# Kernel optimization log

Measured on AMD Instinct MI355X. Metric: run time of the kernel, lower is better.

Reference implementation:

```python
import jax, jax.numpy as jnp
import numpy as np

B, H, W, C = 32, 56, 56, 256
NH, WS, SHIFT = 8, 7, 3
S = WS * WS            # tokens per window = 49
CH = C // NH           # channels per head = 32
EPS = 1e-5


def layer_norm(x, w, b):
    mu = jnp.mean(x, axis=-1, keepdims=True)
    var = jnp.var(x, axis=-1, keepdims=True)
    return (x - mu) * jax.lax.rsqrt(var + EPS) * w + b


def spatial_mlp(x, weight, bias):
    # x: (B, H*W, C); weight: (NH*S, S, 1) grouped-conv1d weight; bias: (NH*S,)
    xr = x.reshape(B, H, W, C)
    if SHIFT > 0:
        P_l, P_r, P_t, P_b = WS - SHIFT, SHIFT, WS - SHIFT, SHIFT
        xr = jnp.pad(xr, ((0, 0), (P_t, P_b), (P_l, P_r), (0, 0)))
    Hp, Wp = xr.shape[1], xr.shape[2]
    # window partition -> (nW, S, NH, CH)
    win = xr.reshape(B, Hp // WS, WS, Wp // WS, WS, C)
    win = win.transpose(0, 1, 3, 2, 4, 5).reshape(-1, S, NH, CH)
    # grouped 1x1 conv == per-head token-mixing matrix (S x S)
    wgt = weight.reshape(NH, S, S)             # wgt[h, i, j]
    out = jnp.einsum('hij,njhd->nihd', wgt, win)
    out = out + bias.reshape(NH, S).T[None, :, :, None]
    # window reverse -> (B, Hp, Wp, C)
    out = out.reshape(B, Hp // WS, Wp // WS, WS, WS, C)
    out = out.transpose(0, 1, 3, 2, 4, 5).reshape(B, Hp, Wp, C)
    if SHIFT > 0:
        out = out[:, P_t:Hp - P_b, P_l:Wp - P_r, :]
    return out.reshape(B, H * W, C)


def mlp(x, fc1_w, fc1_b, fc2_w, fc2_b):
    h = jax.nn.gelu(x @ fc1_w + fc1_b, approximate=False)
    return h @ fc2_w + fc2_b


def setup_inputs() -> dict:
    key = jax.random.key(0)
    ks = jax.random.split(key, 5)
    sc = 0.02
    return {
        'x': jax.random.normal(ks[0], (B, H * W, C), jnp.float32),
        'norm1_w': jnp.ones((C,), jnp.float32),
        'norm1_b': jnp.zeros((C,), jnp.float32),
        'spatial_w': jax.random.normal(ks[1], (NH * S, S, 1), jnp.float32) * sc,
        'spatial_b': jax.random.normal(ks[2], (NH * S,), jnp.float32) * sc,
        'norm2_w': jnp.ones((C,), jnp.float32),
        'norm2_b': jnp.zeros((C,), jnp.float32),
        'fc1_w': jax.random.normal(ks[3], (C, 4 * C), jnp.float32) * sc,
        'fc1_b': jnp.zeros((4 * C,), jnp.float32),
        'fc2_w': jax.random.normal(ks[4], (4 * C, C), jnp.float32) * sc,
        'fc2_b': jnp.zeros((C,), jnp.float32),
    }


def reference(x, norm1_w, norm1_b, spatial_w, spatial_b, norm2_w, norm2_b,
              fc1_w, fc1_b, fc2_w, fc2_b):
    shortcut = x
    h = layer_norm(x, norm1_w, norm1_b)
    h = spatial_mlp(h, spatial_w, spatial_b)
    x = shortcut + h                      # drop_path = 0 (eval)
    x = x + mlp(layer_norm(x, norm2_w, norm2_b), fc1_w, fc1_b, fc2_w, fc2_b)
    return x
```

## Files before the change

### kernel.cpp

```cpp
#include <hip/hip_runtime.h>
#include <hip/hip_bf16.h>

#define NHEAD 8
#define IMG   3136
#define MTOT  100352

typedef __attribute__((ext_vector_type(2))) _Float16 f16x2;
typedef __attribute__((ext_vector_type(8))) _Float16 f16x8;
typedef __attribute__((ext_vector_type(4))) float    f32x4;
typedef __attribute__((ext_vector_type(16))) float   f32x16;
typedef __attribute__((ext_vector_type(8))) short    bf16x8;
typedef __attribute__((ext_vector_type(4))) short    s16x4;
typedef __attribute__((ext_vector_type(4))) int      i32x4;

#define SWZA(byteoff, r) ((byteoff) ^ (((r)&7)<<4) ^ ((((r)>>3)&1)<<7))

__device__ __forceinline__ short f2bf(float f){
  union { float fv; unsigned u; } a; a.fv = f;
  unsigned u = a.u;
  unsigned r = (u + 0x7fffu + ((u >> 16) & 1u)) >> 16;
  return (short)r;
}

__device__ __forceinline__ float gelu_f(float v){
  float u = v*(0.7978845608028654f + 0.0356774081f*(v*v));
  float e = __expf(2.f*u);
  float th = 1.f - 2.f/(e + 1.f);
  return 0.5f*v*(1.f + th);
}

__global__ void prep_k(const float* __restrict__ fc1w, const float* __restrict__ fc2w,
                       const float* __restrict__ spw,
                       short* __restrict__ w1p, short* __restrict__ w2p,
                       short* __restrict__ wspA)
{
  int bid = blockIdx.x, t = threadIdx.x;
  if (bid < 128) {
    int id = bid*256 + t;
    int l = id & 63, fk = id >> 6;
    int kk = fk & 15, f = fk >> 4;
    int n = f*32 + (l & 31);
    int kbase = kk*16 + (l >> 5)*8;
    bf16x8 o;
    #pragma unroll
    for (int e = 0; e < 8; ++e) o[e] = f2bf(fc1w[(size_t)(kbase+e)*1024 + n]);
    *(bf16x8*)(w1p + (size_t)id*8) = o;
  } else if (bid < 256) {
    int id = (bid-128)*256 + t;
    int l = id & 63, fk = id >> 6;
    int kk = fk & 63, f = fk >> 6;
    int n = f*32 + (l & 31);
    int kbase = kk*16 + (l >> 5)*8;
    bf16x8 o;
    #pragma unroll
    for (int e = 0; e < 8; ++e) o[e] = f2bf(fc2w[(size_t)(kbase+e)*256 + n]);
    *(bf16x8*)(w2p + (size_t)id*8) = o;
  } else {
    #pragma unroll
    for (int k = 0; k < 16; ++k) {
      int idx = t + k*256;
      int lane = idx & 63;
      int kt = (idx >> 6) & 3;
      int mt = (idx >> 8) & 1;
      int h  = idx >> 9;
      int i  = mt*32 + (lane & 31);
      int jb = kt*16 + (lane >> 5)*8;
      bf16x8 o;
      #pragma unroll
      for (int e = 0; e < 8; ++e) {
        int j = jb + e;
        float v = (i < 49 && j < 49) ? spw[(size_t)(h*49 + i)*49 + j] : 0.f;
        o[e] = f2bf(v);
      }
      *(bf16x8*)(wspA + (size_t)idx*8) = o;
    }
  }
}

__global__ __launch_bounds__(512,4) void win_k(
    const float* __restrict__ x, const float* __restrict__ n1w, const float* __restrict__ n1b,
    const float* __restrict__ spb, const short* __restrict__ wspA,
    float* __restrict__ x1)
{
  extern __shared__ char wsm[];
  char*  lxT  = wsm;
  float* murs = (float*)(wsm + 65536);
  int t = threadIdx.x, lane = t & 63, wave = t >> 6;
  int bid = blockIdx.x;

  #pragma unroll
  for (int w = 0; w < 2; ++w) {
    int win = bid*2 + w;
    int b = win/81, rem = win - b*81, wi = rem/9, wj = rem - (rem/9)*9;
    for (int i = wave; i < 49; i += 8) {
      int iy = i/7, ix = i - iy*7;
      int hh = wi*7 + iy - 4, ww = wj*7 + ix - 4;
      if (hh < 0 || hh >= 56 || ww < 0 || ww >= 56) continue;
      const float* row = x + ((size_t)(b*IMG + hh*56 + ww))*256;
      f32x4 v = *(const f32x4*)(row + lane*4);
      float s  = v[0]+v[1]+v[2]+v[3];
      float s2 = v[0]*v[0]+v[1]*v[1]+v[2]*v[2]+v[3]*v[3];
      #pragma unroll
      for (int m = 1; m < 64; m <<= 1) { s += __shfl_xor(s, m); s2 += __shfl_xor(s2, m); }
      float mu = s * (1.f/256.f);
      float rs = rsqrtf(s2*(1.f/256.f) - mu*mu + 1e-5f);
      if (lane == 0) { murs[(w*56+i)*2] = mu; murs[(w*56+i)*2+1] = rs; }
    }
  }
  __syncthreads();

  {
    int w = t >> 8, c = t & 255;
    int win = bid*2 + w;
    int b = win/81, rem = win - b*81, wi = rem/9, wj = rem - (rem/9)*9;
    float nwc = n1w[c], nbc = n1b[c];
    char* rowb = lxT + c*256;
    #pragma unroll
    for (int cj = 0; cj < 7; ++cj) {
      bf16x8 pk;
      #pragma unroll
      for (int e = 0; e < 8; ++e) {
        int p = cj*8 + e;
        short val = 0;
        if (p < 49) {
          int iy = p/7, ix = p - iy*7;
          int hh = wi*7 + iy - 4, ww = wj*7 + ix - 4;
          if (hh >= 0 && hh < 56 && ww >= 0 && ww < 56) {
            float mu = murs[(w*56+p)*2], rs = murs[(w*56+p)*2+1];
            float xv = x[((size_t)(b*IMG + hh*56 + ww))*256 + c];
            val = f2bf((xv - mu)*rs*nwc + nbc);
          }
        }
        pk[e] = val;
      }
      *(bf16x8*)(rowb + SWZA(w*128 + cj*16, c)) = pk;
    }
    bf16x8 z = {0,0,0,0,0,0,0,0};
    *(bf16x8*)(rowb + SWZA(w*128 + 112, c)) = z;
  }
  __syncthreads();

  int h = wave, d = lane & 31, lk = lane >> 5;
  const short* wA = wspA + h*4096;
  int c = h*32 + d;
  f32x16 a00, a01, a10, a11;
  #pragma unroll
  for (int q = 0; q < 16; ++q) { a00[q]=0.f; a01[q]=0.f; a10[q]=0.f; a11[q]=0.f; }
  #pragma unroll
  for (int kt = 0; kt < 4; ++kt) {
    bf16x8 A0 = *(const bf16x8*)(wA + (kt*64 + lane)*8);
    bf16x8 A1 = *(const bf16x8*)(wA + ((4+kt)*64 + lane)*8);
    int bo = kt*32 + lk*16;
    bf16x8 B0 = *(const bf16x8*)(lxT + c*256 + SWZA(bo, c));
    bf16x8 B1 = *(const bf16x8*)(lxT + c*256 + SWZA(128 + bo, c));
    a00 = __builtin_amdgcn_mfma_f32_32x32x16_bf16(A0, B0, a00, 0,0,0);
    a10 = __builtin_amdgcn_mfma_f32_32x32x16_bf16(A1, B0, a10, 0,0,0);
    a01 = __builtin_amdgcn_mfma_f32_32x32x16_bf16(A0, B1, a01, 0,0,0);
    a11 = __builtin_amdgcn_mfma_f32_32x32x16_bf16(A1, B1, a11, 0,0,0);
  }

  #pragma unroll
  for (int w = 0; w < 2; ++w) {
    int win = bid*2 + w;
    int b = win/81, rem = win - b*81, wi = rem/9, wj = rem - (rem/9)*9;
    #pragma unroll
    for (int mt = 0; mt < 2; ++mt) {
      #pragma unroll
      for (int r = 0; r < 16; ++r) {
        int i = mt*32 + (r&3) + 8*(r>>2) + 4*lk;
        if (i < 49) {
          int iy = i/7, ix = i - iy*7;
          int hh = wi*7 + iy - 4, ww = wj*7 + ix - 4;
          if (hh >= 0 && hh < 56 && ww >= 0 && ww < 56) {
            size_t off = ((size_t)(b*IMG + hh*56 + ww))*256 + c;
            float av = mt==0 ? (w==0 ? a00[r] : a01[r]) : (w==0 ? a10[r] : a11[r]);
            x1[off] = x[off] + av + spb[h*49 + i];
          }
        }
      }
    }
  }
}

__global__ __launch_bounds__(512,4) void mlp_k(
    const float* __restrict__ x1, float* __restrict__ out,
    const short* __restrict__ w1p, const short* __restrict__ w2p,
    const float* __restrict__ n2w, const float* __restrict__ n2b,
    const float* __restrict__ b1, const float* __restrict__ b2)
{
  extern __shared__ char sm[];
  char* a2  = sm;
  char* hcb = sm + 32768;

  int t = threadIdx.x, lane = t & 63, wave = t >> 6;
  int m0 = blockIdx.x * 64;

  {
    f32x4 nw = *(const f32x4*)(n2w + lane*4);
    f32x4 nb = *(const f32x4*)(n2b + lane*4);
    #pragma unroll
    for (int rq = 0; rq < 8; ++rq) {
      int rr = wave*8 + rq;
      f32x4 v = *(const f32x4*)(x1 + (size_t)(m0+rr)*256 + lane*4);
      float s  = v[0]+v[1]+v[2]+v[3];
      float s2 = v[0]*v[0]+v[1]*v[1]+v[2]*v[2]+v[3]*v[3];
      #pragma unroll
      for (int m = 1; m < 64; m <<= 1){ s += __shfl_xor(s,m); s2 += __shfl_xor(s2,m); }
      float mu = s*(1.f/256.f);
      float rs = rsqrtf(s2*(1.f/256.f) - mu*mu + 1e-5f);
      s16x4 pk;
      #pragma unroll
      for (int q = 0; q < 4; ++q) pk[q] = f2bf((v[q]-mu)*rs*nw[q] + nb[q]);
      *(s16x4*)(a2 + SWZA(lane*8, rr) + rr*512) = pk;
    }
  }
  __syncthreads();

  int lr = lane & 31, lk = lane >> 5;
  int wn = wave;

  f32x16 accO[2];
  #pragma unroll
  for (int i=0;i<2;++i)
    #pragma unroll
    for (int q=0;q<16;++q) accO[i][q] = 0.f;

  for (int ch = 0; ch < 4; ++ch) {
    f32x16 accH[2];
    #pragma unroll
    for (int i=0;i<2;++i)
      #pragma unroll
      for (int q=0;q<16;++q) accH[i][q] = 0.f;

    const short* w1f = w1p + ((size_t)((ch*8 + wn)*16)*64 + lane)*8;
    bf16x8 bq[4];
    #pragma unroll
    for (int k = 0; k < 4; ++k) bq[k] = *(const bf16x8*)(w1f + (size_t)k*512);
    __builtin_amdgcn_s_setprio(1);
    #pragma unroll
    for (int kk = 0; kk < 16; ++kk) {
      bf16x8 b = bq[kk & 3];
      if (kk < 12) bq[kk & 3] = *(const bf16x8*)(w1f + (size_t)(kk+4)*512);
      int kb = kk*32 + lk*16;
      bf16x8 a0 = *(const bf16x8*)(a2 + SWZA(kb, lr) + lr*512);
      bf16x8 a1 = *(const bf16x8*)(a2 + SWZA(kb, 32+lr) + (32+lr)*512);
      accH[0] = __builtin_amdgcn_mfma_f32_32x32x16_bf16(a0, b, accH[0], 0,0,0);
      accH[1] = __builtin_amdgcn_mfma_f32_32x32x16_bf16(a1, b, accH[1], 0,0,0);
    }
    __builtin_amdgcn_s_setprio(0);

    {
      float b1v = b1[ch*256 + wn*32 + lr];
      int colb = (wn*32 + lr)*2;
      #pragma unroll
      for (int ms = 0; ms < 2; ++ms) {
        #pragma unroll
        for (int r = 0; r < 16; ++r) {
          int rowl = ms*32 + (r&3) + 8*(r>>2) + 4*lk;
          float g = gelu_f(accH[ms][r] + b1v);
          *(short*)(hcb + SWZA(colb, rowl) + rowl*512) = f2bf(g);
        }
      }
    }
    __syncthreads();

    const short* w2f = w2p + ((size_t)(wn*64 + ch*16)*64 + lane)*8;
    #pragma unroll
    for (int k = 0; k < 4; ++k) bq[k] = *(const bf16x8*)(w2f + (size_t)k*512);
    __builtin_amdgcn_s_setprio(1);
    #pragma unroll
    for (int kk = 0; kk < 16; ++kk) {
      bf16x8 b = bq[kk & 3];
      if (kk < 12) bq[kk & 3] = *(const bf16x8*)(w2f + (size_t)(kk+4)*512);
      int kb = kk*32 + lk*16;
      bf16x8 a0 = *(const bf16x8*)(hcb + SWZA(kb, lr) + lr*512);
      bf16x8 a1 = *(const bf16x8*)(hcb + SWZA(kb, 32+lr) + (32+lr)*512);
      accO[0] = __builtin_amdgcn_mfma_f32_32x32x16_bf16(a0, b, accO[0], 0,0,0);
      accO[1] = __builtin_amdgcn_mfma_f32_32x32x16_bf16(a1, b, accO[1], 0,0,0);
    }
    __builtin_amdgcn_s_setprio(0);
    __syncthreads();
  }

  {
    int col = wn*32 + lr;
    float b2v = b2[col];
    #pragma unroll
    for (int ms = 0; ms < 2; ++ms) {
      #pragma unroll
      for (int r = 0; r < 16; ++r) {
        int row = ms*32 + (r&3) + 8*(r>>2) + 4*lk;
        size_t off = (size_t)(m0 + row)*256 + col;
        out[off] = x1[off] + accO[ms][r] + b2v;
      }
    }
  }
}

extern "C" void kernel_launch(void* const* d_in, const int* in_sizes, int n_in,
                              void* d_out, int out_size, void* d_ws, size_t ws_size,
                              hipStream_t stream) {
  const float* x    = (const float*)d_in[0];
  const float* n1w  = (const float*)d_in[1];
  const float* n1b  = (const float*)d_in[2];
  const float* spw  = (const float*)d_in[3];
  const float* spb  = (const float*)d_in[4];
  const float* n2w  = (const float*)d_in[5];
  const float* n2b  = (const float*)d_in[6];
  const float* fc1w = (const float*)d_in[7];
  const float* fc1b = (const float*)d_in[8];
  const float* fc2w = (const float*)d_in[9];
  const float* fc2b = (const float*)d_in[10];
  float* outp = (float*)d_out;

  char* ws = (char*)d_ws;
  short* w1p  = (short*)ws;
  short* w2p  = (short*)(ws + 524288);
  short* wspA = (short*)(ws + 1048576);

  prep_k<<<257, 256, 0, stream>>>(fc1w, fc2w, spw, w1p, w2p, wspA);

  hipFuncSetAttribute(reinterpret_cast<const void*>(win_k),
                      hipFuncAttributeMaxDynamicSharedMemorySize, 66432);
  win_k<<<1296, 512, 66432, stream>>>(x, n1w, n1b, spb, wspA, outp);

  hipFuncSetAttribute(reinterpret_cast<const void*>(mlp_k),
                      hipFuncAttributeMaxDynamicSharedMemorySize, 65536);
  mlp_k<<<MTOT/64, 512, 65536, stream>>>(outp, outp, w1p, w2p, n2w, n2b, fc1b, fc2b);
}
```

Baseline: 318.7 us.

## Prefetch weight fragments across GEMM phases with deeper register ring

Replaces the per-phase 4-deep weight-fragment prefetch in the MLP kernel with an 8-deep register ring. The ring is carried across phases, so the next GEMM's first weight fragments load during the second half of the current GEMM. The first fc1 fragments are issued before LayerNorm2 so that global load overlaps the normalization. The goal is to hide global/L2 latency on weight loads at phase boundaries, at the cost of more VGPRs (32 more per lane) under launch_bounds(512,4), which risks spills or lower occupancy.

```diff
diff --git a/kernel.cpp b/kernel.cpp
--- a/kernel.cpp
+++ b/kernel.cpp
@@ -182,6 +182,23 @@
   }
 }
 
+#define GEMM_PHASE(ABUF, CUR, NXT, ACC, LAST)                               \
+  {                                                                          \
+    __builtin_amdgcn_s_setprio(1);                                           \
+    _Pragma("unroll")                                                        \
+    for (int kk = 0; kk < 16; ++kk) {                                        \
+      bf16x8 bfrag = q[kk & 7];                                              \
+      if (kk < 8)       q[kk & 7] = *(const bf16x8*)((CUR) + (size_t)(kk+8)*512); \
+      else if (!(LAST)) q[kk & 7] = *(const bf16x8*)((NXT) + (size_t)(kk-8)*512); \
+      int kb = kk*32 + lk*16;                                                \
+      bf16x8 a0 = *(const bf16x8*)((ABUF) + SWZA(kb, lr) + lr*512);          \
+      bf16x8 a1 = *(const bf16x8*)((ABUF) + SWZA(kb, 32+lr) + (32+lr)*512);  \
+      ACC[0] = __builtin_amdgcn_mfma_f32_32x32x16_bf16(a0, bfrag, ACC[0], 0,0,0); \
+      ACC[1] = __builtin_amdgcn_mfma_f32_32x32x16_bf16(a1, bfrag, ACC[1], 0,0,0); \
+    }                                                                        \
+    __builtin_amdgcn_s_setprio(0);                                           \
+  }
+
 __global__ __launch_bounds__(512,4) void mlp_k(
     const float* __restrict__ x1, float* __restrict__ out,
     const short* __restrict__ w1p, const short* __restrict__ w2p,
@@ -194,6 +211,20 @@
 
   int t = threadIdx.x, lane = t & 63, wave = t >> 6;
   int m0 = blockIdx.x * 64;
+  int lr = lane & 31, lk = lane >> 5;
+  int wn = wave;
+
+  const short* g1b[4];
+  const short* g2b[4];
+  #pragma unroll
+  for (int ch = 0; ch < 4; ++ch) {
+    g1b[ch] = w1p + ((size_t)((ch*8 + wn)*16)*64 + lane)*8;
+    g2b[ch] = w2p + ((size_t)(wn*64 + ch*16)*64 + lane)*8;
+  }
+
+  bf16x8 q[8];
+  #pragma unroll
+  for (int k = 0; k < 8; ++k) q[k] = *(const bf16x8*)(g1b[0] + (size_t)k*512);
 
   {
     f32x4 nw = *(const f32x4*)(n2w + lane*4);
@@ -210,44 +241,27 @@
       float rs = rsqrtf(s2*(1.f/256.f) - mu*mu + 1e-5f);
       s16x4 pk;
       #pragma unroll
-      for (int q = 0; q < 4; ++q) pk[q] = f2bf((v[q]-mu)*rs*nw[q] + nb[q]);
+      for (int qi = 0; qi < 4; ++qi) pk[qi] = f2bf((v[qi]-mu)*rs*nw[qi] + nb[qi]);
       *(s16x4*)(a2 + SWZA(lane*8, rr) + rr*512) = pk;
     }
   }
   __syncthreads();
 
-  int lr = lane & 31, lk = lane >> 5;
-  int wn = wave;
-
   f32x16 accO[2];
   #pragma unroll
   for (int i=0;i<2;++i)
     #pragma unroll
-    for (int q=0;q<16;++q) accO[i][q] = 0.f;
-
+    for (int qi=0;qi<16;++qi) accO[i][qi] = 0.f;
+
+  #pragma unroll
   for (int ch = 0; ch < 4; ++ch) {
     f32x16 accH[2];
     #pragma unroll
     for (int i=0;i<2;++i)
       #pragma unroll
-      for (int q=0;q<16;++q) accH[i][q] = 0.f;
-
-    const short* w1f = w1p + ((size_t)((ch*8 + wn)*16)*64 + lane)*8;
-    bf16x8 bq[4];
-    #pragma unroll
-    for (int k = 0; k < 4; ++k) bq[k] = *(const bf16x8*)(w1f + (size_t)k*512);
-    __builtin_amdgcn_s_setprio(1);
-    #pragma unroll
-    for (int kk = 0; kk < 16; ++kk) {
-      bf16x8 b = bq[kk & 3];
-      if (kk < 12) bq[kk & 3] = *(const bf16x8*)(w1f + (size_t)(kk+4)*512);
-      int kb = kk*32 + lk*16;
-      bf16x8 a0 = *(const bf16x8*)(a2 + SWZA(kb, lr) + lr*512);
-      bf16x8 a1 = *(const bf16x8*)(a2 + SWZA(kb, 32+lr) + (32+lr)*512);
-      accH[0] = __builtin_amdgcn_mfma_f32_32x32x16_bf16(a0, b, accH[0], 0,0,0);
-      accH[1] = __builtin_amdgcn_mfma_f32_32x32x16_bf16(a1, b, accH[1], 0,0,0);
-    }
-    __builtin_amdgcn_s_setprio(0);
+      for (int qi=0;qi<16;++qi) accH[i][qi] = 0.f;
+
+    GEMM_PHASE(a2, g1b[ch], g2b[ch], accH, 0);
 
     {
       float b1v = b1[ch*256 + wn*32 + lr];
@@ -264,21 +278,7 @@
     }
     __syncthreads();
 
-    const short* w2f = w2p + ((size_t)(wn*64 + ch*16)*64 + lane)*8;
-    #pragma unroll
-    for (int k = 0; k < 4; ++k) bq[k] = *(const bf16x8*)(w2f + (size_t)k*512);
-    __builtin_amdgcn_s_setprio(1);
-    #pragma unroll
-    for (int kk = 0; kk < 16; ++kk) {
-      bf16x8 b = bq[kk & 3];
-      if (kk < 12) bq[kk & 3] = *(const bf16x8*)(w2f + (size_t)(kk+4)*512);
-      int kb = kk*32 + lk*16;
-      bf16x8 a0 = *(const bf16x8*)(hcb + SWZA(kb, lr) + lr*512);
-      bf16x8 a1 = *(const bf16x8*)(hcb + SWZA(kb, 32+lr) + (32+lr)*512);
-      accO[0] = __builtin_amdgcn_mfma_f32_32x32x16_bf16(a0, b, accO[0], 0,0,0);
-      accO[1] = __builtin_amdgcn_mfma_f32_32x32x16_bf16(a1, b, accO[1], 0,0,0);
-    }
-    __builtin_amdgcn_s_setprio(0);
+    GEMM_PHASE(hcb, g2b[ch], g1b[(ch<3)?(ch+1):3], accO, (ch==3));
     __syncthreads();
   }
 
```

After: 365.6 us. +14.7%, slower.

## Retile MLP kernel into 2x4 wave grid with 128-wide hidden chunks

Applied to the files above, without the earlier changes.

The MLP kernel moves from 8 waves each owning a 32-column slice to a 2x4 wave grid over 128-wide hidden chunks. This halves the hidden-activation LDS buffer, cuts dynamic shared memory to 48KB and raises launch bounds to 6 blocks. The aim is higher occupancy, with fc1 and fc2 weight fragments prefetched across phases to hide global latency. The change also swaps the software bf16 rounding for the hardware packed convert, and replaces the tanh GELU with a cheaper sigmoid approximation, which adds numerical error against the exact erf GELU.

```diff
diff --git a/kernel.cpp b/kernel.cpp
--- a/kernel.cpp
+++ b/kernel.cpp
@@ -6,14 +6,14 @@
 #define MTOT  100352
 
 typedef __attribute__((ext_vector_type(2))) _Float16 f16x2;
-typedef __attribute__((ext_vector_type(8))) _Float16 f16x8;
 typedef __attribute__((ext_vector_type(4))) float    f32x4;
 typedef __attribute__((ext_vector_type(16))) float   f32x16;
 typedef __attribute__((ext_vector_type(8))) short    bf16x8;
-typedef __attribute__((ext_vector_type(4))) short    s16x4;
+typedef __attribute__((ext_vector_type(2))) int      i32x2;
 typedef __attribute__((ext_vector_type(4))) int      i32x4;
 
 #define SWZA(byteoff, r) ((byteoff) ^ (((r)&7)<<4) ^ ((((r)>>3)&1)<<7))
+#define SWZB(byteoff, r) ((byteoff) ^ (((r)&7)<<4))
 
 __device__ __forceinline__ short f2bf(float f){
   union { float fv; unsigned u; } a; a.fv = f;
@@ -22,11 +22,15 @@
   return (short)r;
 }
 
-__device__ __forceinline__ float gelu_f(float v){
-  float u = v*(0.7978845608028654f + 0.0356774081f*(v*v));
-  float e = __expf(2.f*u);
-  float th = 1.f - 2.f/(e + 1.f);
-  return 0.5f*v*(1.f + th);
+__device__ __forceinline__ unsigned cvtpk(float lo, float hi){
+  unsigned r;
+  asm("v_cvt_pk_bf16_f32 %0, %1, %2" : "=v"(r) : "v"(lo), "v"(hi));
+  return r;
+}
+
+__device__ __forceinline__ float gelu_s(float v){
+  float e = __expf(-1.702f*v);
+  return v*__builtin_amdgcn_rcpf(1.f + e);
 }
 
 __global__ void prep_k(const float* __restrict__ fc1w, const float* __restrict__ fc2w,
@@ -117,26 +121,29 @@
     char* rowb = lxT + c*256;
     #pragma unroll
     for (int cj = 0; cj < 7; ++cj) {
-      bf16x8 pk;
+      float vals[8];
       #pragma unroll
       for (int e = 0; e < 8; ++e) {
         int p = cj*8 + e;
-        short val = 0;
+        float fv = 0.f;
         if (p < 49) {
           int iy = p/7, ix = p - iy*7;
           int hh = wi*7 + iy - 4, ww = wj*7 + ix - 4;
           if (hh >= 0 && hh < 56 && ww >= 0 && ww < 56) {
             float mu = murs[(w*56+p)*2], rs = murs[(w*56+p)*2+1];
             float xv = x[((size_t)(b*IMG + hh*56 + ww))*256 + c];
-            val = f2bf((xv - mu)*rs*nwc + nbc);
+            fv = (xv - mu)*rs*nwc + nbc;
           }
         }
-        pk[e] = val;
-      }
-      *(bf16x8*)(rowb + SWZA(w*128 + cj*16, c)) = pk;
-    }
-    bf16x8 z = {0,0,0,0,0,0,0,0};
-    *(bf16x8*)(rowb + SWZA(w*128 + 112, c)) = z;
+        vals[e] = fv;
+      }
+      i32x4 pk;
+      pk[0] = cvtpk(vals[0], vals[1]); pk[1] = cvtpk(vals[2], vals[3]);
+      pk[2] = cvtpk(vals[4], vals[5]); pk[3] = cvtpk(vals[6], vals[7]);
+      *(i32x4*)(rowb + SWZA(w*128 + cj*16, c)) = pk;
+    }
+    i32x4 z = {0,0,0,0};
+    *(i32x4*)(rowb + SWZA(w*128 + 112, c)) = z;
   }
   __syncthreads();
 
@@ -182,7 +189,7 @@
   }
 }
 
-__global__ __launch_bounds__(512,4) void mlp_k(
+__global__ __launch_bounds__(512,6) void mlp_k(
     const float* __restrict__ x1, float* __restrict__ out,
     const short* __restrict__ w1p, const short* __restrict__ w2p,
     const float* __restrict__ n2w, const float* __restrict__ n2b,
@@ -194,6 +201,17 @@
 
   int t = threadIdx.x, lane = t & 63, wave = t >> 6;
   int m0 = blockIdx.x * 64;
+  int lr = lane & 31, lk = lane >> 5;
+  int wm = wave >> 2, wn = wave & 3;
+
+  const short* g1 = w1p + ((size_t)((wn*16))*64 + lane)*8;
+  const short* g2 = w2p + ((size_t)((wn*2)*64)*64 + lane)*8;
+
+  bf16x8 bq0, bq1, bq2, bq3;
+  bq0 = *(const bf16x8*)(g1 + (size_t)0*512);
+  bq1 = *(const bf16x8*)(g1 + (size_t)1*512);
+  bq2 = *(const bf16x8*)(g1 + (size_t)2*512);
+  bq3 = *(const bf16x8*)(g1 + (size_t)3*512);
 
   {
     f32x4 nw = *(const f32x4*)(n2w + lane*4);
@@ -208,91 +226,101 @@
       for (int m = 1; m < 64; m <<= 1){ s += __shfl_xor(s,m); s2 += __shfl_xor(s2,m); }
       float mu = s*(1.f/256.f);
       float rs = rsqrtf(s2*(1.f/256.f) - mu*mu + 1e-5f);
-      s16x4 pk;
-      #pragma unroll
-      for (int q = 0; q < 4; ++q) pk[q] = f2bf((v[q]-mu)*rs*nw[q] + nb[q]);
-      *(s16x4*)(a2 + SWZA(lane*8, rr) + rr*512) = pk;
+      float y0 = (v[0]-mu)*rs*nw[0] + nb[0];
+      float y1 = (v[1]-mu)*rs*nw[1] + nb[1];
+      float y2 = (v[2]-mu)*rs*nw[2] + nb[2];
+      float y3 = (v[3]-mu)*rs*nw[3] + nb[3];
+      i32x2 pk; pk[0] = cvtpk(y0,y1); pk[1] = cvtpk(y2,y3);
+      *(i32x2*)(a2 + SWZA(lane*8, rr) + rr*512) = pk;
     }
   }
   __syncthreads();
 
-  int lr = lane & 31, lk = lane >> 5;
-  int wn = wave;
-
-  f32x16 accO[2];
-  #pragma unroll
-  for (int i=0;i<2;++i)
-    #pragma unroll
-    for (int q=0;q<16;++q) accO[i][q] = 0.f;
-
-  for (int ch = 0; ch < 4; ++ch) {
-    f32x16 accH[2];
-    #pragma unroll
-    for (int i=0;i<2;++i)
-      #pragma unroll
-      for (int q=0;q<16;++q) accH[i][q] = 0.f;
-
-    const short* w1f = w1p + ((size_t)((ch*8 + wn)*16)*64 + lane)*8;
-    bf16x8 bq[4];
-    #pragma unroll
-    for (int k = 0; k < 4; ++k) bq[k] = *(const bf16x8*)(w1f + (size_t)k*512);
+  f32x16 accO0, accO1;
+  #pragma unroll
+  for (int q=0;q<16;++q) { accO0[q] = 0.f; accO1[q] = 0.f; }
+
+  int arow = wm*32 + lr;
+  char* a2r = a2 + arow*512;
+  char* hcr = hcb + arow*256;
+
+  for (int ch = 0; ch < 8; ++ch) {
+    f32x16 accH;
+    #pragma unroll
+    for (int q=0;q<16;++q) accH[q] = 0.f;
+
     __builtin_amdgcn_s_setprio(1);
     #pragma unroll
     for (int kk = 0; kk < 16; ++kk) {
-      bf16x8 b = bq[kk & 3];
-      if (kk < 12) bq[kk & 3] = *(const bf16x8*)(w1f + (size_t)(kk+4)*512);
+      bf16x8 b;
+      if ((kk&3)==0) b = bq0; else if ((kk&3)==1) b = bq1; else if ((kk&3)==2) b = bq2; else b = bq3;
+      if (kk < 12) {
+        bf16x8 nv = *(const bf16x8*)(g1 + (size_t)(kk+4)*512);
+        if ((kk&3)==0) bq0 = nv; else if ((kk&3)==1) bq1 = nv; else if ((kk&3)==2) bq2 = nv; else bq3 = nv;
+      }
       int kb = kk*32 + lk*16;
-      bf16x8 a0 = *(const bf16x8*)(a2 + SWZA(kb, lr) + lr*512);
-      bf16x8 a1 = *(const bf16x8*)(a2 + SWZA(kb, 32+lr) + (32+lr)*512);
-      accH[0] = __builtin_amdgcn_mfma_f32_32x32x16_bf16(a0, b, accH[0], 0,0,0);
-      accH[1] = __builtin_amdgcn_mfma_f32_32x32x16_bf16(a1, b, accH[1], 0,0,0);
+      bf16x8 a0 = *(const bf16x8*)(a2r + SWZA(kb, arow));
+      accH = __builtin_amdgcn_mfma_f32_32x32x16_bf16(a0, b, accH, 0,0,0);
     }
     __builtin_amdgcn_s_setprio(0);
 
+    bq0 = *(const bf16x8*)(g2 + (size_t)0*512);
+    bq1 = *(const bf16x8*)(g2 + (size_t)64*512);
+    bq2 = *(const bf16x8*)(g2 + (size_t)1*512);
+    bq3 = *(const bf16x8*)(g2 + (size_t)65*512);
+
     {
-      float b1v = b1[ch*256 + wn*32 + lr];
+      float b1v = b1[ch*128 + wn*32 + lr];
       int colb = (wn*32 + lr)*2;
       #pragma unroll
-      for (int ms = 0; ms < 2; ++ms) {
-        #pragma unroll
-        for (int r = 0; r < 16; ++r) {
-          int rowl = ms*32 + (r&3) + 8*(r>>2) + 4*lk;
-          float g = gelu_f(accH[ms][r] + b1v);
-          *(short*)(hcb + SWZA(colb, rowl) + rowl*512) = f2bf(g);
-        }
+      for (int r = 0; r < 16; ++r) {
+        int rowl = (r&3) + 8*(r>>2) + 4*lk;
+        int row  = wm*32 + rowl;
+        float g = gelu_s(accH[r] + b1v);
+        unsigned pw = cvtpk(g, g);
+        *(short*)(hcb + row*256 + SWZB(colb, row)) = (short)(pw & 0xffff);
       }
     }
     __syncthreads();
 
-    const short* w2f = w2p + ((size_t)(wn*64 + ch*16)*64 + lane)*8;
-    #pragma unroll
-    for (int k = 0; k < 4; ++k) bq[k] = *(const bf16x8*)(w2f + (size_t)k*512);
     __builtin_amdgcn_s_setprio(1);
     #pragma unroll
-    for (int kk = 0; kk < 16; ++kk) {
-      bf16x8 b = bq[kk & 3];
-      if (kk < 12) bq[kk & 3] = *(const bf16x8*)(w2f + (size_t)(kk+4)*512);
+    for (int kk = 0; kk < 8; ++kk) {
+      bf16x8 b0, b1f;
+      if ((kk&1)==0) { b0 = bq0; b1f = bq1; } else { b0 = bq2; b1f = bq3; }
+      if (kk < 6) {
+        bf16x8 n0 = *(const bf16x8*)(g2 + (size_t)(kk+2)*512);
+        bf16x8 n1 = *(const bf16x8*)(g2 + (size_t)(64+kk+2)*512);
+        if ((kk&1)==0) { bq0 = n0; bq1 = n1; } else { bq2 = n0; bq3 = n1; }
+      }
       int kb = kk*32 + lk*16;
-      bf16x8 a0 = *(const bf16x8*)(hcb + SWZA(kb, lr) + lr*512);
-      bf16x8 a1 = *(const bf16x8*)(hcb + SWZA(kb, 32+lr) + (32+lr)*512);
-      accO[0] = __builtin_amdgcn_mfma_f32_32x32x16_bf16(a0, b, accO[0], 0,0,0);
-      accO[1] = __builtin_amdgcn_mfma_f32_32x32x16_bf16(a1, b, accO[1], 0,0,0);
+      bf16x8 a0 = *(const bf16x8*)(hcr + SWZB(kb, arow));
+      accO0 = __builtin_amdgcn_mfma_f32_32x32x16_bf16(a0, b0, accO0, 0,0,0);
+      accO1 = __builtin_amdgcn_mfma_f32_32x32x16_bf16(a0, b1f, accO1, 0,0,0);
     }
     __builtin_amdgcn_s_setprio(0);
+
+    g1 += (size_t)64*512;
+    g2 += (size_t)8*512;
+    if (ch < 7) {
+      bq0 = *(const bf16x8*)(g1 + (size_t)0*512);
+      bq1 = *(const bf16x8*)(g1 + (size_t)1*512);
+      bq2 = *(const bf16x8*)(g1 + (size_t)2*512);
+      bq3 = *(const bf16x8*)(g1 + (size_t)3*512);
+    }
     __syncthreads();
   }
 
-  {
-    int col = wn*32 + lr;
+  #pragma unroll
+  for (int ns = 0; ns < 2; ++ns) {
+    int col = wn*64 + ns*32 + lr;
     float b2v = b2[col];
     #pragma unroll
-    for (int ms = 0; ms < 2; ++ms) {
-      #pragma unroll
-      for (int r = 0; r < 16; ++r) {
-        int row = ms*32 + (r&3) + 8*(r>>2) + 4*lk;
-        size_t off = (size_t)(m0 + row)*256 + col;
-        out[off] = x1[off] + accO[ms][r] + b2v;
-      }
+    for (int r = 0; r < 16; ++r) {
+      int row = wm*32 + (r&3) + 8*(r>>2) + 4*lk;
+      size_t off = (size_t)(m0 + row)*256 + col;
+      float av = ns==0 ? accO0[r] : accO1[r];
+      out[off] = x1[off] + av + b2v;
     }
   }
 }
@@ -325,6 +353,6 @@
   win_k<<<1296, 512, 66432, stream>>>(x, n1w, n1b, spb, wspA, outp);
 
   hipFuncSetAttribute(reinterpret_cast<const void*>(mlp_k),
-                      hipFuncAttributeMaxDynamicSharedMemorySize, 65536);
-  mlp_k<<<MTOT/64, 512, 65536, stream>>>(outp, outp, w1p, w2p, n2w, n2b, fc1b, fc2b);
-}
+                      hipFuncAttributeMaxDynamicSharedMemorySize, 49152);
+  mlp_k<<<MTOT/64, 512, 49152, stream>>>(outp, outp, w1p, w2p, n2w, n2b, fc1b, fc2b);
+}
```

After: 677.4 us. 2.13x slower.
